# Kernel optimization log

Hardware: AMD Instinct MI355X
Metric: run time of the kernel (lower is better)

Reference implementation:

```python
import jax, jax.numpy as jnp
import numpy as np

B, D, NTXT, H = 16384, 512, 4096, 1024


def _linear_params(key, fan_in, fan_out):
    kw, kb = jax.random.split(key)
    s = 1.0 / np.sqrt(fan_in)
    W = jax.random.uniform(kw, (fan_in, fan_out), jnp.float32, -s, s)
    b = jax.random.uniform(kb, (fan_out,), jnp.float32, -s, s)
    return W, b


def setup_inputs() -> dict:
    key = jax.random.key(0)
    ks = jax.random.split(key, 9)
    img_features = jax.random.normal(ks[0], (B, D), jnp.float32)
    txt_features = jax.random.normal(ks[1], (D, NTXT), jnp.float32)
    target_ind = jax.random.randint(ks[2], (B,), 0, NTXT, jnp.int32)
    Wi0, bi0 = _linear_params(ks[3], D, H)
    Wi1, bi1 = _linear_params(ks[4], H, H)
    Wi2, bi2 = _linear_params(ks[5], H, D)
    Wt0, bt0 = _linear_params(ks[6], D, H)
    Wt1, bt1 = _linear_params(ks[7], H, H)
    Wt2, bt2 = _linear_params(ks[8], H, D)
    logit_scale = jnp.asarray(np.log(1.0 / 0.07), jnp.float32)
    temp = jnp.asarray(1.0, jnp.float32)
    return {
        "img_features": img_features, "txt_features": txt_features,
        "target_ind": target_ind, "temp": temp,
        "Wi0": Wi0, "bi0": bi0, "Wi1": Wi1, "bi1": bi1, "Wi2": Wi2, "bi2": bi2,
        "Wt0": Wt0, "bt0": bt0, "Wt1": Wt1, "bt1": bt1, "Wt2": Wt2, "bt2": bt2,
        "logit_scale": logit_scale,
    }


def _mlp(x, params):
    # ReLU after every layer except the last (matches MLP.forward)
    for W, b in params[:-1]:
        x = jax.nn.relu(x @ W + b)
    W, b = params[-1]
    return x @ W + b


def reference(img_features, txt_features, target_ind, temp,
              Wi0, bi0, Wi1, bi1, Wi2, bi2,
              Wt0, bt0, Wt1, bt1, Wt2, bt2, logit_scale):
    p_img = _mlp(img_features, [(Wi0, bi0), (Wi1, bi1), (Wi2, bi2)])          # [B, D]
    p_txt = _mlp(txt_features.T, [(Wt0, bt0), (Wt1, bt1), (Wt2, bt2)])        # [N, D]

    sim = (p_img @ p_txt.T) * jnp.exp(logit_scale)                            # [B, N]
    sim = sim / jnp.linalg.norm(sim, axis=-1, keepdims=True)
    out_logits = sim / jnp.linalg.norm(sim, axis=-1, keepdims=True)           # faithful double-normalize

    # vectorized form of the per-sample Python-loop softmax-CE in MLP_CLIP_loss
    logp = jax.nn.log_softmax(out_logits / temp, axis=-1)                     # [B, N]
    picked = jnp.take_along_axis(logp, target_ind[:, None].astype(jnp.int32), axis=1)[:, 0]
    loss = -jnp.mean(picked)

    # accuracy branch (uses unscaled similarity, row-normalized)
    sim_clip = p_img @ p_txt.T
    sim_clip = sim_clip / jnp.linalg.norm(sim_clip, axis=-1, keepdims=True)
    acc = jnp.sum(jnp.argmax(sim_clip, axis=1).astype(jnp.int32) == target_ind)
    return loss, acc
```

## Files before the change

kernel.cpp:

```cpp
#include <hip/hip_runtime.h>
#include <cstdint>
#include <cstddef>

#define B_ROWS 16384
#define D_DIM  512
#define NTXT_N 4096
#define H_DIM  1024

typedef __attribute__((ext_vector_type(8))) short short8;
typedef __attribute__((ext_vector_type(4))) float f32x4;

__device__ __forceinline__ ushort f2bf(float x) {
    union { float f; uint32_t u; } c; c.f = x;
    const uint32_t u = c.u;
    return (ushort)((u + 0x7fffu + ((u >> 16) & 1u)) >> 16);
}
__device__ __forceinline__ float bf2f(ushort h) {
    union { uint32_t u; float f; } c; c.u = ((uint32_t)h) << 16;
    return c.f;
}

#define GLDS16(gp, lp) __builtin_amdgcn_global_load_lds( \
    (const __attribute__((address_space(1))) void*)(gp),  \
    (__attribute__((address_space(3))) void*)(lp), 16, 0, 0)

__device__ __forceinline__ void xcd_remap(int& bx, int& by) {
    const int nx = gridDim.x, ny = gridDim.y;
    const int nwg = nx * ny;
    const int bid = by * nx + bx;
    const int q = nwg >> 3, r = nwg & 7;
    const int xcd = bid & 7, idx = bid >> 3;
    const int nb = (xcd < r ? xcd * (q + 1) : r * (q + 1) + (xcd - r) * q) + idx;
    bx = nb % nx; by = nb / nx;
}

__global__ void init_kernel(int* acc) {
    if (threadIdx.x == 0 && blockIdx.x == 0) *acc = 0;
}

__global__ void tsplit_kernel(const float* __restrict__ in, ushort* __restrict__ oh,
                              ushort* __restrict__ ol, int R, int C, int cbase)
{
    __shared__ float tile[32][33];
    const int c0 = blockIdx.x * 32, r0 = blockIdx.y * 32;
    const int tx = threadIdx.x, ty = threadIdx.y;
    #pragma unroll
    for (int j = 0; j < 32; j += 8)
        tile[ty + j][tx] = in[(size_t)(r0 + ty + j) * C + cbase + c0 + tx];
    __syncthreads();
    #pragma unroll
    for (int j = 0; j < 32; j += 8) {
        const float v = tile[tx][ty + j];
        const ushort h = f2bf(v);
        const size_t idx = (size_t)(c0 + ty + j) * R + r0 + tx;
        oh[idx] = h;
        ol[idx] = f2bf(v - bf2f(h));
    }
}

__global__ void csplit_kernel(const float* __restrict__ in, ushort* __restrict__ oh,
                              ushort* __restrict__ ol, int n)
{
    const int i = (blockIdx.x * 256 + threadIdx.x) * 4;
    if (i >= n) return;
    const float4 f = *(const float4*)&in[i];
    ushort4 h, l;
    h.x = f2bf(f.x); l.x = f2bf(f.x - bf2f(h.x));
    h.y = f2bf(f.y); l.y = f2bf(f.y - bf2f(h.y));
    h.z = f2bf(f.z); l.z = f2bf(f.z - bf2f(h.z));
    h.w = f2bf(f.w); l.w = f2bf(f.w - bf2f(h.w));
    *(ushort4*)&oh[i] = h;
    *(ushort4*)&ol[i] = l;
}

template<int K, int OMODE, bool RELU, bool BIAS>
__global__ __launch_bounds__(256, 2)
void gemm3_kernel(const ushort* __restrict__ Ah, const ushort* __restrict__ Al,
                  const ushort* __restrict__ Bh, const ushort* __restrict__ Bl,
                  const float* __restrict__ bias,
                  float* __restrict__ Cf, ushort* __restrict__ Ch, ushort* __restrict__ Cl,
                  int M, int N)
{
    constexpr int SEG = K / 32;
    constexpr int NT  = 3 * SEG;

    __shared__ __align__(16) ushort LDSB[3 * 8192];

    const int tid  = threadIdx.x;
    const int lane = tid & 63;
    const int w    = tid >> 6;
    const int wr   = w >> 1, wc = w & 1;

    int bxi = blockIdx.x, byi = blockIdx.y;
    xcd_remap(bxi, byi);
    const int bm = byi * 128, bn = bxi * 128;

    const int    stlo  = w * 1024;
    const int    srow  = w * 32 + (lane >> 2);
    const int    scol  = (((lane & 3) ^ ((lane >> 3) & 3)) << 3);
    const size_t aoff0 = (size_t)(bm + srow) * K + scol;
    const size_t boff0 = (size_t)(bn + srow) * K + scol;

    const int frow  = lane & 15;
    const int koff  = ((lane >> 4) ^ ((frow >> 1) & 3)) << 3;

    f32x4 acc[4][4];
    #pragma unroll
    for (int m = 0; m < 4; ++m)
        #pragma unroll
        for (int n = 0; n < 4; ++n)
            acc[m][n] = (f32x4)0.0f;

#define STAGE_ISSUE(sidx) do {                                                \
        const int _s = (sidx);                                                \
        const int _seg = _s / SEG;                                            \
        const int _kk  = (_s - _seg * SEG) * 32;                              \
        const ushort* _ap = (_seg == 2 ? Al : Ah) + aoff0 + _kk;              \
        const ushort* _bp = (_seg == 1 ? Bl : Bh) + boff0 + _kk;              \
        ushort* _ab = &LDSB[(_s % 3) * 8192];                                 \
        ushort* _bb = _ab + 4096;                                             \
        GLDS16(_ap,              _ab + stlo);                                 \
        GLDS16(_ap + 16 * K,     _ab + stlo + 512);                           \
        GLDS16(_bp,              _bb + stlo);                                 \
        GLDS16(_bp + 16 * K,     _bb + stlo + 512);                           \
    } while (0)

#define COMPUTE(bi) do {                                                      \
        const ushort* _As = &LDSB[(bi) * 8192];                               \
        const ushort* _Bs = _As + 4096;                                       \
        short8 _af[4], _bf[4];                                                \
        _Pragma("unroll")                                                     \
        for (int m = 0; m < 4; ++m)                                           \
            _af[m] = *(const short8*)&_As[(wr * 64 + m * 16 + frow) * 32 + koff]; \
        _Pragma("unroll")                                                     \
        for (int n = 0; n < 4; ++n)                                           \
            _bf[n] = *(const short8*)&_Bs[(wc * 64 + n * 16 + frow) * 32 + koff]; \
        __builtin_amdgcn_s_setprio(1);                                        \
        _Pragma("unroll")                                                     \
        for (int m = 0; m < 4; ++m)                                           \
            _Pragma("unroll")                                                 \
            for (int n = 0; n < 4; ++n)                                       \
                acc[m][n] = __builtin_amdgcn_mfma_f32_16x16x32_bf16(          \
                    _af[m], _bf[n], acc[m][n], 0, 0, 0);                      \
        __builtin_amdgcn_s_setprio(0);                                        \
    } while (0)

#define WAITV4  asm volatile("s_waitcnt vmcnt(4)" ::: "memory")
#define WAITV0  asm volatile("s_waitcnt vmcnt(0)" ::: "memory")
#define BARRIER asm volatile("s_barrier" ::: "memory")

    STAGE_ISSUE(0);
    STAGE_ISSUE(1);

    int t = 0;
    for (int trip = 0; trip < NT / 3 - 1; ++trip, t += 3) {
        WAITV4; BARRIER; STAGE_ISSUE(t + 2); COMPUTE(0);
        WAITV4; BARRIER; STAGE_ISSUE(t + 3); COMPUTE(1);
        WAITV4; BARRIER; STAGE_ISSUE(t + 4); COMPUTE(2);
    }
    WAITV4; BARRIER; STAGE_ISSUE(NT - 1); COMPUTE(0);
    WAITV4; BARRIER;                      COMPUTE(1);
    WAITV0; BARRIER;                      COMPUTE(2);

#undef STAGE_ISSUE
#undef COMPUTE
#undef WAITV4
#undef WAITV0
#undef BARRIER

    const int crow0 = bm + wr * 64 + (lane >> 4) * 4;
    const int ccol0 = bn + wc * 64 + (lane & 15);
    #pragma unroll
    for (int m = 0; m < 4; ++m)
        #pragma unroll
        for (int n = 0; n < 4; ++n) {
            const int col = ccol0 + n * 16;
            const float bv = BIAS ? bias[col] : 0.0f;
            #pragma unroll
            for (int q = 0; q < 4; ++q) {
                float v = acc[m][n][q] + bv;
                if (RELU) v = fmaxf(v, 0.0f);
                const size_t idx = (size_t)(crow0 + m * 16 + q) * N + col;
                if (OMODE == 0) {
                    Cf[idx] = v;
                } else {
                    const ushort h = f2bf(v);
                    Ch[idx] = h;
                    Cl[idx] = f2bf(v - bf2f(h));
                }
            }
        }
}

__global__ __launch_bounds__(256) void rowreduce_kernel(
    const float* __restrict__ sim, const int* __restrict__ tgt,
    const float* __restrict__ temp_p, float* __restrict__ perrow,
    int* __restrict__ acc_cnt, int row0)
{
    const int row = blockIdx.x;
    const float* srow = sim + (size_t)row * NTXT_N;
    const int tid = threadIdx.x;

    float v[16];
    #pragma unroll
    for (int q = 0; q < 4; ++q) {
        float4 f = *(const float4*)&srow[4 * tid + 1024 * q];
        v[4 * q + 0] = f.x; v[4 * q + 1] = f.y; v[4 * q + 2] = f.z; v[4 * q + 3] = f.w;
    }

    float ss = 0.0f, mx = -3.4e38f; int mi = 0x7fffffff;
    #pragma unroll
    for (int q = 0; q < 4; ++q)
        #pragma unroll
        for (int r = 0; r < 4; ++r) {
            const int j = 4 * tid + 1024 * q + r;
            const float x = v[4 * q + r];
            ss = fmaf(x, x, ss);
            if (x > mx) { mx = x; mi = j; }
            else if (x == mx && j < mi) mi = j;
        }

    #pragma unroll
    for (int off = 32; off; off >>= 1) {
        ss += __shfl_down(ss, off);
        const float omx = __shfl_down(mx, off);
        const int   omi = __shfl_down(mi, off);
        if (omx > mx || (omx == mx && omi < mi)) { mx = omx; mi = omi; }
    }

    __shared__ float sws[4], swm[4];
    __shared__ int   swi[4];
    __shared__ float bC, bMx;
    __shared__ int   bAmax;
    const int w = tid >> 6, lane = tid & 63;
    if (lane == 0) { sws[w] = ss; swm[w] = mx; swi[w] = mi; }
    __syncthreads();
    if (tid == 0) {
        float tss = 0.0f, tmx = -3.4e38f; int tmi = 0x7fffffff;
        #pragma unroll
        for (int i = 0; i < 4; ++i) {
            tss += sws[i];
            if (swm[i] > tmx || (swm[i] == tmx && swi[i] < tmi)) { tmx = swm[i]; tmi = swi[i]; }
        }
        const float inv_nr = 1.0f / sqrtf(tss);
        const float n2 = sqrtf(tss * inv_nr * inv_nr);
        const float Cv = inv_nr / (n2 * temp_p[0]);
        bC = Cv; bMx = tmx * Cv; bAmax = tmi;
    }
    __syncthreads();
    const float Cv = bC, mxx = bMx;

    float es = 0.0f;
    #pragma unroll
    for (int q = 0; q < 16; ++q) es += expf(v[q] * Cv - mxx);
    #pragma unroll
    for (int off = 32; off; off >>= 1) es += __shfl_down(es, off);
    if (lane == 0) sws[w] = es;
    __syncthreads();
    if (tid == 0) {
        const float tes = sws[0] + sws[1] + sws[2] + sws[3];
        const float lse = mxx + logf(tes);
        const int t = tgt[row0 + row];
        perrow[row0 + row] = lse - srow[t] * Cv;
        if (bAmax == t) atomicAdd(acc_cnt, 1);
    }
}

__global__ __launch_bounds__(256) void finalize_kernel(
    const float* __restrict__ perrow, const int* __restrict__ acc_cnt,
    float* __restrict__ out)
{
    __shared__ float red[256];
    const int tid = threadIdx.x;
    float s = 0.0f;
    for (int i = tid; i < B_ROWS; i += 256) s += perrow[i];
    red[tid] = s;
    __syncthreads();
    for (int st = 128; st; st >>= 1) {
        if (tid < st) red[tid] += red[tid + st];
        __syncthreads();
    }
    if (tid == 0) {
        out[0] = red[0] / (float)B_ROWS;
        out[1] = (float)(*acc_cnt);
    }
}

extern "C" void kernel_launch(void* const* d_in, const int* in_sizes, int n_in,
                              void* d_out, int out_size, void* d_ws, size_t ws_size,
                              hipStream_t stream)
{
    const float* img  = (const float*)d_in[0];
    const float* txt  = (const float*)d_in[1];
    const int*   tgt  = (const int*)  d_in[2];
    const float* temp = (const float*)d_in[3];
    const float* Wf[6] = { (const float*)d_in[4],  (const float*)d_in[6],  (const float*)d_in[8],
                           (const float*)d_in[10], (const float*)d_in[12], (const float*)d_in[14] };
    const float* bf[6] = { (const float*)d_in[5],  (const float*)d_in[7],  (const float*)d_in[9],
                           (const float*)d_in[11], (const float*)d_in[13], (const float*)d_in[15] };
    float* out = (float*)d_out;

    const int wK[6] = { D_DIM, H_DIM, H_DIM, D_DIM, H_DIM, H_DIM };
    const int wN[6] = { H_DIM, H_DIM, D_DIM, H_DIM, H_DIM, D_DIM };

    auto need = [&](size_t ch, size_t sc) -> size_t {
        size_t wt = 0;
        for (int i = 0; i < 6; ++i) wt += (size_t)wK[i] * wN[i] * 2 * 2;
        const size_t a01 = 2 * (ch * H_DIM * 2 * 2);
        const size_t pt  = (size_t)NTXT_N * D_DIM * 2 * 2;
        const size_t sim = sc * NTXT_N * 4;
        return wt + a01 + pt + sim + (size_t)B_ROWS * 4 + (size_t)64 * 1024;
    };
    const size_t ladder[][2] = { {16384, 4096}, {16384, 2048}, {8192, 4096}, {8192, 2048},
                                 {4096, 2048},  {4096, 1024},  {2048, 1024}, {1024, 1024} };
    size_t CH = 1024, SIMCH = 512;
    for (auto& e : ladder)
        if (need(e[0], e[1]) <= ws_size) { CH = e[0]; SIMCH = e[1]; break; }

    uint8_t* p = (uint8_t*)d_ws;
    auto alloc = [&](size_t bytes) -> void* {
        void* r = (void*)p; p += (bytes + 255) & ~(size_t)255; return r;
    };
    ushort* WTh[6]; ushort* WTl[6];
    for (int i = 0; i < 6; ++i) {
        WTh[i] = (ushort*)alloc((size_t)wK[i] * wN[i] * 2);
        WTl[i] = (ushort*)alloc((size_t)wK[i] * wN[i] * 2);
    }
    ushort* A0h = (ushort*)alloc(CH * H_DIM * 2);
    ushort* A0l = (ushort*)alloc(CH * H_DIM * 2);
    ushort* A1h = (ushort*)alloc(CH * H_DIM * 2);
    ushort* A1l = (ushort*)alloc(CH * H_DIM * 2);
    ushort* PTh = (ushort*)alloc((size_t)NTXT_N * D_DIM * 2);
    ushort* PTl = (ushort*)alloc((size_t)NTXT_N * D_DIM * 2);
    float*  SIM = (float*)alloc(SIMCH * NTXT_N * 4);
    float*  PERROW = (float*)alloc((size_t)B_ROWS * 4);
    int*    ACC = (int*)alloc(64);
    ushort* XBh = A1h;  ushort* XBl = A1l;
    ushort* PIh = A0h;  ushort* PIl = A0l;

    init_kernel<<<1, 64, 0, stream>>>(ACC);

    for (int i = 0; i < 6; ++i)
        tsplit_kernel<<<dim3(wN[i] / 32, wK[i] / 32), dim3(32, 8), 0, stream>>>(
            Wf[i], WTh[i], WTl[i], wK[i], wN[i], 0);

    const size_t CHT = CH < (size_t)NTXT_N ? CH : (size_t)NTXT_N;
    for (size_t n0 = 0; n0 < NTXT_N; n0 += CHT) {
        tsplit_kernel<<<dim3(CHT / 32, D_DIM / 32), dim3(32, 8), 0, stream>>>(
            txt, XBh, XBl, D_DIM, NTXT_N, (int)n0);
        gemm3_kernel<D_DIM, 1, true, true><<<dim3(H_DIM / 128, CHT / 128), 256, 0, stream>>>(
            XBh, XBl, WTh[3], WTl[3], bf[3], nullptr, A0h, A0l, (int)CHT, H_DIM);
        gemm3_kernel<H_DIM, 1, true, true><<<dim3(H_DIM / 128, CHT / 128), 256, 0, stream>>>(
            A0h, A0l, WTh[4], WTl[4], bf[4], nullptr, A1h, A1l, (int)CHT, H_DIM);
        gemm3_kernel<H_DIM, 1, false, true><<<dim3(D_DIM / 128, CHT / 128), 256, 0, stream>>>(
            A1h, A1l, WTh[5], WTl[5], bf[5], nullptr,
            PTh + n0 * D_DIM, PTl + n0 * D_DIM, (int)CHT, D_DIM);
    }

    for (size_t m0 = 0; m0 < B_ROWS; m0 += CH) {
        csplit_kernel<<<(CH * D_DIM / 4 + 255) / 256, 256, 0, stream>>>(
            img + m0 * D_DIM, XBh, XBl, (int)(CH * D_DIM));
        gemm3_kernel<D_DIM, 1, true, true><<<dim3(H_DIM / 128, CH / 128), 256, 0, stream>>>(
            XBh, XBl, WTh[0], WTl[0], bf[0], nullptr, A0h, A0l, (int)CH, H_DIM);
        gemm3_kernel<H_DIM, 1, true, true><<<dim3(H_DIM / 128, CH / 128), 256, 0, stream>>>(
            A0h, A0l, WTh[1], WTl[1], bf[1], nullptr, A1h, A1l, (int)CH, H_DIM);
        gemm3_kernel<H_DIM, 1, false, true><<<dim3(D_DIM / 128, CH / 128), 256, 0, stream>>>(
            A1h, A1l, WTh[2], WTl[2], bf[2], nullptr, PIh, PIl, (int)CH, D_DIM);
        for (size_t s0 = 0; s0 < CH; s0 += SIMCH) {
            gemm3_kernel<D_DIM, 0, false, false><<<dim3(NTXT_N / 128, SIMCH / 128), 256, 0, stream>>>(
                PIh + s0 * D_DIM, PIl + s0 * D_DIM, PTh, PTl, nullptr,
                SIM, nullptr, nullptr, (int)SIMCH, NTXT_N);
            rowreduce_kernel<<<SIMCH, 256, 0, stream>>>(
                SIM, tgt, temp, PERROW, ACC, (int)(m0 + s0));
        }
    }

    finalize_kernel<<<1, 256, 0, stream>>>(PERROW, ACC, out);
}
```

Before: 793.2 us.

## Fuse three bf16 split passes into one K loop with double buffering

Replaces the GEMM that streamed the three split-precision products (hi*hi, hi*lo, lo*hi) as separate K segments with one that loads all four hi/lo tiles per K step and issues the three MFMAs back to back on each accumulator. The K loop becomes one third as long and each A/B tile is fetched once per step instead of once per segment, which cuts global loads and barriers. The pipeline goes from a 3-stage ring using raw vmcnt waits to a 2-buffer scheme with __syncthreads. LDS per block rises from 48KB to 64KB, and the plain syncthreads drains outstanding loads, so overlap between load and compute may be lower and occupancy may drop.

```diff
diff --git a/kernel.cpp b/kernel.cpp
--- a/kernel.cpp
+++ b/kernel.cpp
@@ -75,16 +75,14 @@
 
 template<int K, int OMODE, bool RELU, bool BIAS>
 __global__ __launch_bounds__(256, 2)
-void gemm3_kernel(const ushort* __restrict__ Ah, const ushort* __restrict__ Al,
-                  const ushort* __restrict__ Bh, const ushort* __restrict__ Bl,
-                  const float* __restrict__ bias,
-                  float* __restrict__ Cf, ushort* __restrict__ Ch, ushort* __restrict__ Cl,
-                  int M, int N)
-{
-    constexpr int SEG = K / 32;
-    constexpr int NT  = 3 * SEG;
-
-    __shared__ __align__(16) ushort LDSB[3 * 8192];
+void gemm_p2_kernel(const ushort* __restrict__ Ah, const ushort* __restrict__ Al,
+                    const ushort* __restrict__ Bh, const ushort* __restrict__ Bl,
+                    const float* __restrict__ bias,
+                    float* __restrict__ Cf, ushort* __restrict__ Ch, ushort* __restrict__ Cl,
+                    int M, int N)
+{
+    constexpr int NT = K / 32;
+    __shared__ __align__(16) ushort LDSB[2 * 4 * 4096];
 
     const int tid  = threadIdx.x;
     const int lane = tid & 63;
@@ -101,8 +99,8 @@
     const size_t aoff0 = (size_t)(bm + srow) * K + scol;
     const size_t boff0 = (size_t)(bn + srow) * K + scol;
 
-    const int frow  = lane & 15;
-    const int koff  = ((lane >> 4) ^ ((frow >> 1) & 3)) << 3;
+    const int frow = lane & 15;
+    const int koff = ((lane >> 4) ^ ((frow >> 1) & 3)) << 3;
 
     f32x4 acc[4][4];
     #pragma unroll
@@ -111,62 +109,62 @@
         for (int n = 0; n < 4; ++n)
             acc[m][n] = (f32x4)0.0f;
 
-#define STAGE_ISSUE(sidx) do {                                                \
-        const int _s = (sidx);                                                \
-        const int _seg = _s / SEG;                                            \
-        const int _kk  = (_s - _seg * SEG) * 32;                              \
-        const ushort* _ap = (_seg == 2 ? Al : Ah) + aoff0 + _kk;              \
-        const ushort* _bp = (_seg == 1 ? Bl : Bh) + boff0 + _kk;              \
-        ushort* _ab = &LDSB[(_s % 3) * 8192];                                 \
-        ushort* _bb = _ab + 4096;                                             \
-        GLDS16(_ap,              _ab + stlo);                                 \
-        GLDS16(_ap + 16 * K,     _ab + stlo + 512);                           \
-        GLDS16(_bp,              _bb + stlo);                                 \
-        GLDS16(_bp + 16 * K,     _bb + stlo + 512);                           \
+#define STAGE(tt, bi) do {                                                    \
+        const int _kk = (tt) * 32;                                            \
+        ushort* _b = &LDSB[(bi) * 16384];                                     \
+        GLDS16(Ah + aoff0 + _kk,          _b +         stlo);                 \
+        GLDS16(Ah + aoff0 + _kk + 16 * K, _b +         stlo + 512);           \
+        GLDS16(Al + aoff0 + _kk,          _b +  4096 + stlo);                 \
+        GLDS16(Al + aoff0 + _kk + 16 * K, _b +  4096 + stlo + 512);           \
+        GLDS16(Bh + boff0 + _kk,          _b +  8192 + stlo);                 \
+        GLDS16(Bh + boff0 + _kk + 16 * K, _b +  8192 + stlo + 512);           \
+        GLDS16(Bl + boff0 + _kk,          _b + 12288 + stlo);                 \
+        GLDS16(Bl + boff0 + _kk + 16 * K, _b + 12288 + stlo + 512);           \
     } while (0)
 
 #define COMPUTE(bi) do {                                                      \
-        const ushort* _As = &LDSB[(bi) * 8192];                               \
-        const ushort* _Bs = _As + 4096;                                       \
-        short8 _af[4], _bf[4];                                                \
+        const ushort* _Ahs = &LDSB[(bi) * 16384];                             \
+        const ushort* _Als = _Ahs + 4096;                                     \
+        const ushort* _Bhs = _Ahs + 8192;                                     \
+        const ushort* _Bls = _Ahs + 12288;                                    \
+        short8 a_h[4], a_l[4], b_h[4], b_l[4];                                \
         _Pragma("unroll")                                                     \
-        for (int m = 0; m < 4; ++m)                                           \
-            _af[m] = *(const short8*)&_As[(wr * 64 + m * 16 + frow) * 32 + koff]; \
+        for (int m = 0; m < 4; ++m) {                                         \
+            const int off = (wr * 64 + m * 16 + frow) * 32 + koff;            \
+            a_h[m] = *(const short8*)&_Ahs[off];                              \
+            a_l[m] = *(const short8*)&_Als[off];                              \
+        }                                                                     \
         _Pragma("unroll")                                                     \
-        for (int n = 0; n < 4; ++n)                                           \
-            _bf[n] = *(const short8*)&_Bs[(wc * 64 + n * 16 + frow) * 32 + koff]; \
+        for (int n = 0; n < 4; ++n) {                                         \
+            const int off = (wc * 64 + n * 16 + frow) * 32 + koff;            \
+            b_h[n] = *(const short8*)&_Bhs[off];                              \
+            b_l[n] = *(const short8*)&_Bls[off];                              \
+        }                                                                     \
         __builtin_amdgcn_s_setprio(1);                                        \
         _Pragma("unroll")                                                     \
         for (int m = 0; m < 4; ++m)                                           \
             _Pragma("unroll")                                                 \
-            for (int n = 0; n < 4; ++n)                                       \
+            for (int n = 0; n < 4; ++n) {                                     \
                 acc[m][n] = __builtin_amdgcn_mfma_f32_16x16x32_bf16(          \
-                    _af[m], _bf[n], acc[m][n], 0, 0, 0);                      \
+                    a_h[m], b_h[n], acc[m][n], 0, 0, 0);                      \
+                acc[m][n] = __builtin_amdgcn_mfma_f32_16x16x32_bf16(          \
+                    a_h[m], b_l[n], acc[m][n], 0, 0, 0);                      \
+                acc[m][n] = __builtin_amdgcn_mfma_f32_16x16x32_bf16(          \
+                    a_l[m], b_h[n], acc[m][n], 0, 0, 0);                      \
+            }                                                                 \
         __builtin_amdgcn_s_setprio(0);                                        \
     } while (0)
 
-#define WAITV4  asm volatile("s_waitcnt vmcnt(4)" ::: "memory")
-#define WAITV0  asm volatile("s_waitcnt vmcnt(0)" ::: "memory")
-#define BARRIER asm volatile("s_barrier" ::: "memory")
-
-    STAGE_ISSUE(0);
-    STAGE_ISSUE(1);
-
-    int t = 0;
-    for (int trip = 0; trip < NT / 3 - 1; ++trip, t += 3) {
-        WAITV4; BARRIER; STAGE_ISSUE(t + 2); COMPUTE(0);
-        WAITV4; BARRIER; STAGE_ISSUE(t + 3); COMPUTE(1);
-        WAITV4; BARRIER; STAGE_ISSUE(t + 4); COMPUTE(2);
-    }
-    WAITV4; BARRIER; STAGE_ISSUE(NT - 1); COMPUTE(0);
-    WAITV4; BARRIER;                      COMPUTE(1);
-    WAITV0; BARRIER;                      COMPUTE(2);
-
-#undef STAGE_ISSUE
+    STAGE(0, 0);
+    #pragma unroll 2
+    for (int t = 0; t < NT; ++t) {
+        __syncthreads();
+        if (t + 1 < NT) STAGE(t + 1, (t + 1) & 1);
+        COMPUTE(t & 1);
+    }
+
+#undef STAGE
 #undef COMPUTE
-#undef WAITV4
-#undef WAITV0
-#undef BARRIER
 
     const int crow0 = bm + wr * 64 + (lane >> 4) * 4;
     const int ccol0 = bn + wc * 64 + (lane & 15);
@@ -348,11 +346,11 @@
     for (size_t n0 = 0; n0 < NTXT_N; n0 += CHT) {
         tsplit_kernel<<<dim3(CHT / 32, D_DIM / 32), dim3(32, 8), 0, stream>>>(
             txt, XBh, XBl, D_DIM, NTXT_N, (int)n0);
-        gemm3_kernel<D_DIM, 1, true, true><<<dim3(H_DIM / 128, CHT / 128), 256, 0, stream>>>(
+        gemm_p2_kernel<D_DIM, 1, true, true><<<dim3(H_DIM / 128, CHT / 128), 256, 0, stream>>>(
             XBh, XBl, WTh[3], WTl[3], bf[3], nullptr, A0h, A0l, (int)CHT, H_DIM);
-        gemm3_kernel<H_DIM, 1, true, true><<<dim3(H_DIM / 128, CHT / 128), 256, 0, stream>>>(
+        gemm_p2_kernel<H_DIM, 1, true, true><<<dim3(H_DIM / 128, CHT / 128), 256, 0, stream>>>(
             A0h, A0l, WTh[4], WTl[4], bf[4], nullptr, A1h, A1l, (int)CHT, H_DIM);
-        gemm3_kernel<H_DIM, 1, false, true><<<dim3(D_DIM / 128, CHT / 128), 256, 0, stream>>>(
+        gemm_p2_kernel<H_DIM, 1, false, true><<<dim3(D_DIM / 128, CHT / 128), 256, 0, stream>>>(
             A1h, A1l, WTh[5], WTl[5], bf[5], nullptr,
             PTh + n0 * D_DIM, PTl + n0 * D_DIM, (int)CHT, D_DIM);
     }
@@ -360,14 +358,14 @@
     for (size_t m0 = 0; m0 < B_ROWS; m0 += CH) {
         csplit_kernel<<<(CH * D_DIM / 4 + 255) / 256, 256, 0, stream>>>(
             img + m0 * D_DIM, XBh, XBl, (int)(CH * D_DIM));
-        gemm3_kernel<D_DIM, 1, true, true><<<dim3(H_DIM / 128, CH / 128), 256, 0, stream>>>(
+        gemm_p2_kernel<D_DIM, 1, true, true><<<dim3(H_DIM / 128, CH / 128), 256, 0, stream>>>(
             XBh, XBl, WTh[0], WTl[0], bf[0], nullptr, A0h, A0l, (int)CH, H_DIM);
-        gemm3_kernel<H_DIM, 1, true, true><<<dim3(H_DIM / 128, CH / 128), 256, 0, stream>>>(
+        gemm_p2_kernel<H_DIM, 1, true, true><<<dim3(H_DIM / 128, CH / 128), 256, 0, stream>>>(
             A0h, A0l, WTh[1], WTl[1], bf[1], nullptr, A1h, A1l, (int)CH, H_DIM);
-        gemm3_kernel<H_DIM, 1, false, true><<<dim3(D_DIM / 128, CH / 128), 256, 0, stream>>>(
+        gemm_p2_kernel<H_DIM, 1, false, true><<<dim3(D_DIM / 128, CH / 128), 256, 0, stream>>>(
             A1h, A1l, WTh[2], WTl[2], bf[2], nullptr, PIh, PIl, (int)CH, D_DIM);
         for (size_t s0 = 0; s0 < CH; s0 += SIMCH) {
-            gemm3_kernel<D_DIM, 0, false, false><<<dim3(NTXT_N / 128, SIMCH / 128), 256, 0, stream>>>(
+            gemm_p2_kernel<D_DIM, 0, false, false><<<dim3(NTXT_N / 128, SIMCH / 128), 256, 0, stream>>>(
                 PIh + s0 * D_DIM, PIl + s0 * D_DIM, PTh, PTl, nullptr,
                 SIM, nullptr, nullptr, (int)SIMCH, NTXT_N);
             rowreduce_kernel<<<SIMCH, 256, 0, stream>>>(
```

After: 706.0 us. -11.0%, faster.
